# Performance work log

Measured on AMD Instinct MI355X. Metric: run time of the kernel, lower is better.

## Reference

```python
import jax, jax.numpy as jnp
import numpy as np
import math

C = 256
N_HEAD = 8
GROUPS = 16
EPS = 1e-5


def group_norm(x, w, b):
    # x: [B, C, H, W]; biased variance over (group_channels, H, W), like torch GroupNorm
    B, Cc, H, W = x.shape
    xg = x.reshape(B, GROUPS, Cc // GROUPS, H, W)
    mean = xg.mean(axis=(2, 3, 4), keepdims=True)
    var = ((xg - mean) ** 2).mean(axis=(2, 3, 4), keepdims=True)
    xn = ((xg - mean) * jax.lax.rsqrt(var + EPS)).reshape(B, Cc, H, W)
    return xn * w[None, :, None, None] + b[None, :, None, None]


def setup_inputs() -> dict:
    key = jax.random.key(0)
    k0, k1, k2, k3, k4, k5 = jax.random.split(key, 6)
    B, H, W = 4, 48, 48
    input_feat = jax.random.normal(k0, (B, C, H, W), dtype=jnp.float32)
    gn_weight = jnp.ones((C,), dtype=jnp.float32) + 0.02 * jax.random.normal(k1, (C,), dtype=jnp.float32)
    gn_bias = 0.02 * jax.random.normal(k2, (C,), dtype=jnp.float32)
    w_qkv = jax.random.normal(k3, (3 * C, C), dtype=jnp.float32) / math.sqrt(C)  # Conv2d 1x1, no bias
    w_out = jax.random.normal(k4, (C, C), dtype=jnp.float32) / math.sqrt(C)      # Conv2d 1x1
    b_out = 0.02 * jax.random.normal(k5, (C,), dtype=jnp.float32)
    return {"input_feat": input_feat, "gn_weight": gn_weight, "gn_bias": gn_bias,
            "w_qkv": w_qkv, "w_out": w_out, "b_out": b_out}


def reference(input_feat, gn_weight, gn_bias, w_qkv, w_out, b_out):
    # H=W=48 <= max_attn_size=48 -> full attention branch
    B, Cc, H, W = input_feat.shape
    n, d = N_HEAD, Cc // N_HEAD
    S = H * W
    normed = group_norm(input_feat, gn_weight, gn_bias)
    # 1x1 conv QKV: [B, 3C, H, W]
    qkv = jnp.einsum('oc,bchw->bohw', w_qkv, normed)
    # view(B, n, 3*d, H, W).chunk(3, dim=2) == reshape to (B, n, 3, d, S)
    qkv = qkv.reshape(B, n, 3, d, S)
    q, k, v = qkv[:, :, 0], qkv[:, :, 1], qkv[:, :, 2]  # each [B, n, d, S]
    # NOTE: original divides by sqrt(channel), not sqrt(head_dim)
    scale = 1.0 / math.sqrt(Cc)
    scores = jnp.einsum('bnds,bndt->bnst', q, k) * scale  # [B, n, S, S]
    attn = jax.nn.softmax(scores, axis=-1)
    o = jnp.einsum('bnst,bndt->bnds', attn, v)  # [B, n, d, S]
    o = o.reshape(B, Cc, H, W)
    out = jnp.einsum('oc,bchw->bohw', w_out, o) + b_out[None, :, None, None]
    return out + input_feat
```

## Files before the change

### kernel.cpp

```cpp
#include <hip/hip_runtime.h>
#include <hip/hip_bf16.h>
#include <stdint.h>

#define S    2304
#define CHN  256
#define BATCH 4
#define NKEYS 1152
#define QS   0.09016844005556021f

typedef __attribute__((ext_vector_type(8))) short bf16x8;
typedef __attribute__((ext_vector_type(4))) short bf16x4;
typedef __attribute__((ext_vector_type(4))) float f32x4;
typedef __attribute__((ext_vector_type(4))) uint32_t u32x4;
typedef __attribute__((ext_vector_type(4))) unsigned short u16x4;
typedef unsigned short u16;

#define AS1 __attribute__((address_space(1)))
#define AS3 __attribute__((address_space(3)))
#define GLDS(gptr, lptr) __builtin_amdgcn_global_load_lds((const AS1 void*)(gptr), (AS3 void*)(lptr), 16, 0, 0)

__device__ __forceinline__ u16 f2bf(float f) {
  union { float f; uint32_t u; } v; v.f = f;
  uint32_t u = v.u;
  u += 0x7fffu + ((u >> 16) & 1u);
  return (u16)(u >> 16);
}
__device__ __forceinline__ float bf2f(u16 h) {
  union { uint32_t u; float f; } v; v.u = ((uint32_t)h) << 16;
  return v.f;
}
__device__ __forceinline__ uint32_t pk_bf16(float a, float b) {
  union { __hip_bfloat162 h; uint32_t u; } cv;
  cv.h = __float22bfloat162_rn(make_float2(a, b));
  return cv.u;
}

__global__ void k_prep(const float* __restrict__ wq, const float* __restrict__ wo,
                       u16* __restrict__ wq_bf, u16* __restrict__ wo_bf,
                       float* __restrict__ sraw) {
  int i = blockIdx.x * 256 + threadIdx.x;
  if (blockIdx.x == 0 && threadIdx.x < 128) sraw[threadIdx.x] = 0.f;
  if (i < 768 * 256) wq_bf[i] = f2bf(wq[i]);
  int j = i - 768 * 256;
  if (j >= 0 && j < 256 * 256) wo_bf[j] = f2bf(wo[j]);
}

__global__ void k_gnstats(const float* __restrict__ x, float* __restrict__ sraw) {
  int blk = blockIdx.x;
  int bg = blk >> 2, part = blk & 3;
  const float4* p = (const float4*)(x + (size_t)bg * 36864) + part * 2304;
  float s = 0.f, ss = 0.f;
  for (int i = threadIdx.x; i < 2304; i += 256) {
    float4 v = p[i];
    s  += v.x + v.y + v.z + v.w;
    ss += v.x * v.x + v.y * v.y + v.z * v.z + v.w * v.w;
  }
  int lane = threadIdx.x & 63, wv = threadIdx.x >> 6;
  for (int m = 1; m < 64; m <<= 1) { s += __shfl_xor(s, m, 64); ss += __shfl_xor(ss, m, 64); }
  __shared__ float rs[4], rss[4];
  if (lane == 0) { rs[wv] = s; rss[wv] = ss; }
  __syncthreads();
  if (threadIdx.x == 0) {
    float S_ = rs[0] + rs[1] + rs[2] + rs[3];
    float SS = rss[0] + rss[1] + rss[2] + rss[3];
    atomicAdd(&sraw[bg * 2], S_);
    atomicAdd(&sraw[bg * 2 + 1], SS);
  }
}

__global__ void k_gnnorm(const float* __restrict__ x, const float* __restrict__ w,
                         const float* __restrict__ bias, const float* __restrict__ sraw,
                         u16* __restrict__ nt) {
  int bid = blockIdx.x;
  int b = bid / 144, r = bid % 144;
  int sblk = r >> 2, cq = r & 3;
  int t = threadIdx.x;
  int ni = t & 63, cgrp = t >> 6;
  int s = sblk * 64 + ni;
  int cbase = cq * 64 + cgrp * 16;
  int bgi = b * 16 + (cbase >> 4);
  float sx = sraw[bgi * 2], ssx = sraw[bgi * 2 + 1];
  float mean = sx * (1.f / 36864.f);
  float var  = ssx * (1.f / 36864.f) - mean * mean;
  float rstd = rsqrtf(var + 1e-5f);
  bf16x8 v0, v1;
  #pragma unroll
  for (int e = 0; e < 16; ++e) {
    int c = cbase + e;
    float val = x[(size_t)(b * 256 + c) * S + s];
    float xn = (val - mean) * rstd * w[c] + bias[c];
    if (e < 8) v0[e] = (short)f2bf(xn); else v1[e - 8] = (short)f2bf(xn);
  }
  u16* dst = nt + (size_t)(b * S + s) * 256 + cbase;
  *(bf16x8*)dst = v0;
  *(bf16x8*)(dst + 8) = v1;
}

__global__ __launch_bounds__(256) void k_qkv(const u16* __restrict__ A,
                                             const u16* __restrict__ Bm,
                                             u16* __restrict__ qkt,
                                             u16* __restrict__ vt) {
  __shared__ __align__(16) u16 As[2][64 * 32];
  __shared__ __align__(16) u16 Bs[2][128 * 32];
  int tid = threadIdx.x, lane = tid & 63, w = tid >> 6;
  int wr = w >> 1, wc = w & 1;
  int cb = lane & 15, q4 = lane >> 4;
  int m0 = blockIdx.y * 64, n0 = blockIdx.x * 128;

  const u16* gA0 = A  + (size_t)(m0 + (tid >> 2)) * 256 + (tid & 3) * 8;
  const u16* gB0 = Bm + (size_t)(n0 + (tid >> 2)) * 256 + (tid & 3) * 8;
  const u16* gB1 = gB0 + 64 * 256;
  char* lA = (char*)&As[0][0] + (w << 10);
  char* lB = (char*)&Bs[0][0] + (w << 10);

  #define STAGE_Q(buf, k0) do {                      \
    GLDS(gA0 + (k0), lA + (buf) * 4096);             \
    GLDS(gB0 + (k0), lB + (buf) * 8192);             \
    GLDS(gB1 + (k0), lB + (buf) * 8192 + 4096);      \
  } while (0)

  f32x4 zero4 = {0.f, 0.f, 0.f, 0.f};
  f32x4 acc[2][4];
  for (int i = 0; i < 2; ++i) for (int j = 0; j < 4; ++j) acc[i][j] = zero4;

  STAGE_Q(0, 0);
  __syncthreads();
  for (int ks = 0; ks < 8; ++ks) {
    int cur = ks & 1;
    if (ks < 7) STAGE_Q(cur ^ 1, (ks + 1) * 32);
    const u16* as = &As[cur][0];
    const u16* bs = &Bs[cur][0];
    bf16x8 af[2], bfr[4];
    for (int i = 0; i < 2; ++i)
      af[i]  = *(const bf16x8*)&as[(wr * 32 + i * 16 + cb) * 32 + 8 * q4];
    for (int j = 0; j < 4; ++j)
      bfr[j] = *(const bf16x8*)&bs[(wc * 64 + j * 16 + cb) * 32 + 8 * q4];
    for (int i = 0; i < 2; ++i)
      for (int j = 0; j < 4; ++j)
        acc[i][j] = __builtin_amdgcn_mfma_f32_16x16x32_bf16(af[i], bfr[j], acc[i][j], 0, 0, 0);
    __syncthreads();
  }

  for (int i = 0; i < 2; ++i)
    for (int j = 0; j < 4; ++j) {
      int ob = m0 + wr * 32 + i * 16 + q4 * 4;
      int n  = n0 + wc * 64 + j * 16 + cb;
      int h = ob / 96, oq = ob % 96;
      if (oq < 64) {
        float sc = (oq < 32) ? QS : 1.f;
        u16x4 pk;
        for (int r = 0; r < 4; ++r) pk[r] = f2bf(acc[i][j][r] * sc);
        *(u16x4*)&qkt[(size_t)n * 512 + h * 64 + oq] = pk;
      } else {
        for (int r = 0; r < 4; ++r)
          vt[(size_t)(h * 32 + oq - 64 + r) * 9216 + n] = f2bf(acc[i][j][r]);
      }
    }
  #undef STAGE_Q
}

__global__ __launch_bounds__(512) void k_attn(const u16* __restrict__ qkt,
                                              const u16* __restrict__ vt,
                                              u16* __restrict__ ot) {
  __shared__ __align__(16) u16 Ks[2][2][2048];
  __shared__ __align__(16) u16 Vd[2][2][2048];
  __shared__ float Ls[8][16];

  int tid = threadIdx.x, lane = tid & 63, w = tid >> 6;
  int cb = lane & 15, g4 = lane >> 4;
  int qw = w & 3, half = w >> 2;
  int hw = blockIdx.x;
  int orig = (hw & 7) * 144 + (hw >> 3);
  int bh = orig / 36, qtile = orig % 36;
  int b = bh >> 3, h = bh & 7;
  int q0 = qtile * 64 + qw * 16;

  const u16* kbase = qkt + (size_t)(b * S) * 512 + h * 64 + 32 + (size_t)half * NKEYS * 512;
  const u16* vbase = vt + (size_t)(h * 32) * 9216 + (size_t)b * S + half * NKEYS;

  bf16x8 qf = *(const bf16x8*)&qkt[(size_t)(b * S + q0 + cb) * 512 + h * 64 + 8 * g4];
  bf16x8 vones;
  #pragma unroll
  for (int e = 0; e < 8; ++e) vones[e] = (short)0x3F80;

  f32x4 zero4 = {0.f, 0.f, 0.f, 0.f};
  f32x4 acc_o[2]; acc_o[0] = zero4; acc_o[1] = zero4;
  f32x4 lacc4 = zero4;

  int xk = (cb ^ (cb >> 2)) & 3;

  const u16* p_k = &Ks[half][0][cb * 32 + ((g4 ^ xk) * 8)];
  const u16* p_v[2][2];
  #pragma unroll
  for (int kk = 0; kk < 2; ++kk)
    #pragma unroll
    for (int h2 = 0; h2 < 2; ++h2) {
      int chunk = 4 * kk + 2 * h2 + (g4 >> 1);
      p_v[kk][h2] = &Vd[half][0][cb * 64 + ((chunk ^ (cb & 7)) << 3) + 4 * (g4 & 1)];
    }

  int tloc = tid & 255;
  int krow = tloc >> 2, kch = (tloc & 3) ^ ((krow ^ (krow >> 2)) & 3);
  int vrow = tloc >> 3, vch = (tloc & 7) ^ (vrow & 7);
  const u16* gK = kbase + (size_t)krow * 512 + kch * 8;
  const u16* gV = vbase + (size_t)vrow * 9216 + vch * 8;
  char* ldsK = (char*)&Ks[half][0][0] + (qw << 10);
  char* ldsV = (char*)&Vd[half][0][0] + (qw << 10);

  #define STAGE_A(buf) do {                          \
    GLDS(gK, ldsK + (buf) * 4096);                   \
    GLDS(gV, ldsV + (buf) * 4096);                   \
    gK += 64 * 512; gV += 64;                        \
  } while (0)

  #define TILE(buf, pf) do {                                                   \
    if (pf) STAGE_A(buf ^ 1);                                                  \
    bf16x8 kf[4];                                                              \
    _Pragma("unroll")                                                          \
    for (int k4 = 0; k4 < 4; ++k4)                                             \
      kf[k4] = *(const bf16x8*)(p_k + (buf) * 2048 + k4 * 512);                \
    bf16x4 vlo[2][2], vhi[2][2];                                 \
    _Pragma("unroll")                                                          \
    for (int jd = 0; jd < 2; ++jd)                                             \
      _Pragma("unroll")                                                        \
      for (int kk = 0; kk < 2; ++kk) {                                         \
        vlo[jd][kk] = *(const bf16x4*)(p_v[kk][0] + (buf) * 2048 + jd * 1024); \
        vhi[jd][kk] = *(const bf16x4*)(p_v[kk][1] + (buf) * 2048 + jd * 1024); \
      }                                                                        \
    f32x4 pacc[4];                                                             \
    __builtin_amdgcn_s_setprio(1);                                             \
    _Pragma("unroll")                                                          \
    for (int k4 = 0; k4 < 4; ++k4)                                             \
      pacc[k4] = __builtin_amdgcn_mfma_f32_16x16x32_bf16(kf[k4], qf, zero4, 0, 0, 0); \
    __builtin_amdgcn_s_setprio(0);                                             \
    uint32_t W01[4], W23[4];                                                   \
    _Pragma("unroll")                                                          \
    for (int k4 = 0; k4 < 4; ++k4) {                                           \
      f32x4 p = pacc[k4];                                                      \
      float e0 = __builtin_amdgcn_exp2f(p[0]);                                 \
      float e1 = __builtin_amdgcn_exp2f(p[1]);                                 \
      float e2 = __builtin_amdgcn_exp2f(p[2]);                                 \
      float e3 = __builtin_amdgcn_exp2f(p[3]);                                 \
      W01[k4] = pk_bf16(e0, e1);                                               \
      W23[k4] = pk_bf16(e2, e3);                                               \
    }                                                                          \
    union { u32x4 u; bf16x8 v; } pu0, pu1;                                     \
    pu0.u = (u32x4){W01[0], W23[0], W01[1], W23[1]};                           \
    pu1.u = (u32x4){W01[2], W23[2], W01[3], W23[3]};                           \
    __builtin_amdgcn_s_setprio(1);                                             \
    lacc4 = __builtin_amdgcn_mfma_f32_16x16x32_bf16(pu0.v, vones, lacc4, 0, 0, 0); \
    lacc4 = __builtin_amdgcn_mfma_f32_16x16x32_bf16(pu1.v, vones, lacc4, 0, 0, 0); \
    _Pragma("unroll")                                                          \
    for (int jd = 0; jd < 2; ++jd) {                                           \
      bf16x8 vb0 = __builtin_shufflevector(vlo[jd][0], vhi[jd][0], 0,1,2,3,4,5,6,7); \
      bf16x8 vb1 = __builtin_shufflevector(vlo[jd][1], vhi[jd][1], 0,1,2,3,4,5,6,7); \
      acc_o[jd] = __builtin_amdgcn_mfma_f32_16x16x32_bf16(pu0.v, vb0, acc_o[jd], 0, 0, 0); \
      acc_o[jd] = __builtin_amdgcn_mfma_f32_16x16x32_bf16(pu1.v, vb1, acc_o[jd], 0, 0, 0); \
    }                                                                          \
    __builtin_amdgcn_s_setprio(0);                                             \
    __syncthreads();                                                           \
  } while (0)

  STAGE_A(0);
  __syncthreads();
  for (int it = 0; it < 9; ++it) {
    TILE(0, 1);
    TILE(1, it < 8);
  }

  float* OsF = (float*)&Ks[0][0][0];
  float* myO = OsF + w * 512;
  #pragma unroll
  for (int jd = 0; jd < 2; ++jd)
    *(f32x4*)&myO[(cb + 16 * jd) * 16 + 4 * g4] = acc_o[jd];
  if (cb == 0)
    *(f32x4*)&Ls[w][4 * g4] = lacc4;
  __syncthreads();

  const float* A0 = OsF + qw * 512;
  const float* A1 = OsF + (qw + 4) * 512;
  int dd = half * 16 + cb;
  f32x4 s0 = *(const f32x4*)&A0[dd * 16 + 4 * g4];
  f32x4 s1 = *(const f32x4*)&A1[dd * 16 + 4 * g4];
  f32x4 lt0 = *(const f32x4*)&Ls[qw][4 * g4];
  f32x4 lt1 = *(const f32x4*)&Ls[qw + 4][4 * g4];
  #pragma unroll
  for (int r = 0; r < 4; ++r) {
    float inv = __builtin_amdgcn_rcpf(lt0[r] + lt1[r]);
    int sq = q0 + 4 * g4 + r;
    ot[(size_t)(b * S + sq) * 256 + h * 32 + dd] = f2bf((s0[r] + s1[r]) * inv);
  }
  #undef STAGE_A
  #undef TILE
}

__global__ __launch_bounds__(256) void k_oproj(const u16* __restrict__ A,
                                               const u16* __restrict__ Bm,
                                               float* __restrict__ out,
                                               const float* __restrict__ bias,
                                               const float* __restrict__ resid) {
  __shared__ __align__(16) u16 As[2][64 * 32];
  __shared__ __align__(16) u16 Bs[2][64 * 32];
  int tid = threadIdx.x, lane = tid & 63, w = tid >> 6;
  int cb = lane & 15, q4 = lane >> 4;
  int m0 = blockIdx.y * 64, n0 = blockIdx.x * 64;

  const u16* gA0 = A  + (size_t)(m0 + (tid >> 2)) * 256 + (tid & 3) * 8;
  const u16* gB0 = Bm + (size_t)(n0 + (tid >> 2)) * 256 + (tid & 3) * 8;
  char* lA = (char*)&As[0][0] + (w << 10);
  char* lB = (char*)&Bs[0][0] + (w << 10);

  #define STAGE_O(buf, k0) do {                      \
    GLDS(gA0 + (k0), lA + (buf) * 4096);             \
    GLDS(gB0 + (k0), lB + (buf) * 4096);             \
  } while (0)

  f32x4 zero4 = {0.f, 0.f, 0.f, 0.f};
  f32x4 acc[4];
  for (int j = 0; j < 4; ++j) acc[j] = zero4;

  STAGE_O(0, 0);
  __syncthreads();
  for (int ks = 0; ks < 8; ++ks) {
    int cur = ks & 1;
    if (ks < 7) STAGE_O(cur ^ 1, (ks + 1) * 32);
    const u16* as = &As[cur][0];
    const u16* bs = &Bs[cur][0];
    bf16x8 af = *(const bf16x8*)&as[(w * 16 + cb) * 32 + 8 * q4];
    bf16x8 bfr[4];
    for (int j = 0; j < 4; ++j)
      bfr[j] = *(const bf16x8*)&bs[(j * 16 + cb) * 32 + 8 * q4];
    for (int j = 0; j < 4; ++j)
      acc[j] = __builtin_amdgcn_mfma_f32_16x16x32_bf16(af, bfr[j], acc[j], 0, 0, 0);
    __syncthreads();
  }

  for (int j = 0; j < 4; ++j)
    for (int r = 0; r < 4; ++r) {
      int o = m0 + w * 16 + q4 * 4 + r;
      int n = n0 + j * 16 + cb;
      int b = n / S, s2 = n % S;
      size_t gi = (size_t)(b * 256 + o) * S + s2;
      out[gi] = acc[j][r] + bias[o] + resid[gi];
    }
  #undef STAGE_O
}

extern "C" void kernel_launch(void* const* d_in, const int* in_sizes, int n_in,
                              void* d_out, int out_size, void* d_ws, size_t ws_size,
                              hipStream_t stream) {
  const float* input = (const float*)d_in[0];
  const float* gnw   = (const float*)d_in[1];
  const float* gnb   = (const float*)d_in[2];
  const float* wqkv  = (const float*)d_in[3];
  const float* wout  = (const float*)d_in[4];
  const float* bout  = (const float*)d_in[5];
  float* out = (float*)d_out;
  char* ws = (char*)d_ws;

  size_t o_wq  = 0;
  size_t o_wo  = o_wq + (size_t)768 * 256 * 2;
  size_t o_st  = o_wo + (size_t)256 * 256 * 2;
  size_t o_nt  = o_st + 1024;
  size_t o_qkt = o_nt + (size_t)9216 * 256 * 2;
  size_t o_vt  = o_qkt + (size_t)9216 * 512 * 2;

  u16*    wq_bf = (u16*)(ws + o_wq);
  u16*    wo_bf = (u16*)(ws + o_wo);
  float*  sraw  = (float*)(ws + o_st);
  u16*    nt    = (u16*)(ws + o_nt);
  u16*    qkt   = (u16*)(ws + o_qkt);
  u16*    vt    = (u16*)(ws + o_vt);
  u16*    otb   = (u16*)(ws + o_nt);

  k_prep<<<1024, 256, 0, stream>>>(wqkv, wout, wq_bf, wo_bf, sraw);
  k_gnstats<<<256, 256, 0, stream>>>(input, sraw);
  k_gnnorm<<<576, 256, 0, stream>>>(input, gnw, gnb, sraw, nt);
  k_qkv<<<dim3(72, 12), 256, 0, stream>>>(wq_bf, nt, qkt, vt);
  k_attn<<<1152, 512, 0, stream>>>(qkt, vt, otb);
  k_oproj<<<dim3(144, 4), 256, 0, stream>>>(wo_bf, otb, out, bout, input);
}
```

Before: 88.03 us.

## Drop intra-block key split in attention kernel, use 256-thread blocks

The attention kernel no longer splits the key range across two halves of a 512-thread block. Each 256-thread block now walks all 2304 keys itself, which removes the LDS partial-sum exchange, the extra barrier and the final combine step. The kernel runs twice as many tile iterations per wave and asks for higher occupancy through launch bounds (256, 8). The trade-off is less parallelism per query tile and a longer serial loop, in exchange for less LDS use and simpler synchronisation.

Result: slower. 90.28 us (+2.6%).

```diff
diff --git a/kernel.cpp b/kernel.cpp
--- a/kernel.cpp
+++ b/kernel.cpp
@@ -5,7 +5,6 @@
 #define S    2304
 #define CHN  256
 #define BATCH 4
-#define NKEYS 1152
 #define QS   0.09016844005556021f
 
 typedef __attribute__((ext_vector_type(8))) short bf16x8;
@@ -159,24 +158,22 @@
   #undef STAGE_Q
 }
 
-__global__ __launch_bounds__(512) void k_attn(const u16* __restrict__ qkt,
-                                              const u16* __restrict__ vt,
-                                              u16* __restrict__ ot) {
-  __shared__ __align__(16) u16 Ks[2][2][2048];
-  __shared__ __align__(16) u16 Vd[2][2][2048];
-  __shared__ float Ls[8][16];
+__global__ __launch_bounds__(256, 8) void k_attn(const u16* __restrict__ qkt,
+                                                 const u16* __restrict__ vt,
+                                                 u16* __restrict__ ot) {
+  __shared__ __align__(16) u16 Ks[2][2048];
+  __shared__ __align__(16) u16 Vd[2][2048];
 
   int tid = threadIdx.x, lane = tid & 63, w = tid >> 6;
   int cb = lane & 15, g4 = lane >> 4;
-  int qw = w & 3, half = w >> 2;
   int hw = blockIdx.x;
   int orig = (hw & 7) * 144 + (hw >> 3);
   int bh = orig / 36, qtile = orig % 36;
   int b = bh >> 3, h = bh & 7;
-  int q0 = qtile * 64 + qw * 16;
-
-  const u16* kbase = qkt + (size_t)(b * S) * 512 + h * 64 + 32 + (size_t)half * NKEYS * 512;
-  const u16* vbase = vt + (size_t)(h * 32) * 9216 + (size_t)b * S + half * NKEYS;
+  int q0 = qtile * 64 + w * 16;
+
+  const u16* kbase = qkt + (size_t)(b * S) * 512 + h * 64 + 32;
+  const u16* vbase = vt + (size_t)(h * 32) * 9216 + (size_t)b * S;
 
   bf16x8 qf = *(const bf16x8*)&qkt[(size_t)(b * S + q0 + cb) * 512 + h * 64 + 8 * g4];
   bf16x8 vones;
@@ -189,23 +186,22 @@
 
   int xk = (cb ^ (cb >> 2)) & 3;
 
-  const u16* p_k = &Ks[half][0][cb * 32 + ((g4 ^ xk) * 8)];
+  const u16* p_k = &Ks[0][cb * 32 + ((g4 ^ xk) * 8)];
   const u16* p_v[2][2];
   #pragma unroll
   for (int kk = 0; kk < 2; ++kk)
     #pragma unroll
     for (int h2 = 0; h2 < 2; ++h2) {
       int chunk = 4 * kk + 2 * h2 + (g4 >> 1);
-      p_v[kk][h2] = &Vd[half][0][cb * 64 + ((chunk ^ (cb & 7)) << 3) + 4 * (g4 & 1)];
+      p_v[kk][h2] = &Vd[0][cb * 64 + ((chunk ^ (cb & 7)) << 3) + 4 * (g4 & 1)];
     }
 
-  int tloc = tid & 255;
-  int krow = tloc >> 2, kch = (tloc & 3) ^ ((krow ^ (krow >> 2)) & 3);
-  int vrow = tloc >> 3, vch = (tloc & 7) ^ (vrow & 7);
+  int krow = tid >> 2, kch = (tid & 3) ^ ((krow ^ (krow >> 2)) & 3);
+  int vrow = tid >> 3, vch = (tid & 7) ^ (vrow & 7);
   const u16* gK = kbase + (size_t)krow * 512 + kch * 8;
   const u16* gV = vbase + (size_t)vrow * 9216 + vch * 8;
-  char* ldsK = (char*)&Ks[half][0][0] + (qw << 10);
-  char* ldsV = (char*)&Vd[half][0][0] + (qw << 10);
+  char* ldsK = (char*)&Ks[0][0] + (w << 10);
+  char* ldsV = (char*)&Vd[0][0] + (w << 10);
 
   #define STAGE_A(buf) do {                          \
     GLDS(gK, ldsK + (buf) * 4096);                   \
@@ -263,32 +259,18 @@
 
   STAGE_A(0);
   __syncthreads();
-  for (int it = 0; it < 9; ++it) {
+  for (int it = 0; it < 18; ++it) {
     TILE(0, 1);
-    TILE(1, it < 8);
-  }
-
-  float* OsF = (float*)&Ks[0][0][0];
-  float* myO = OsF + w * 512;
-  #pragma unroll
-  for (int jd = 0; jd < 2; ++jd)
-    *(f32x4*)&myO[(cb + 16 * jd) * 16 + 4 * g4] = acc_o[jd];
-  if (cb == 0)
-    *(f32x4*)&Ls[w][4 * g4] = lacc4;
-  __syncthreads();
-
-  const float* A0 = OsF + qw * 512;
-  const float* A1 = OsF + (qw + 4) * 512;
-  int dd = half * 16 + cb;
-  f32x4 s0 = *(const f32x4*)&A0[dd * 16 + 4 * g4];
-  f32x4 s1 = *(const f32x4*)&A1[dd * 16 + 4 * g4];
-  f32x4 lt0 = *(const f32x4*)&Ls[qw][4 * g4];
-  f32x4 lt1 = *(const f32x4*)&Ls[qw + 4][4 * g4];
+    TILE(1, it < 17);
+  }
+
   #pragma unroll
   for (int r = 0; r < 4; ++r) {
-    float inv = __builtin_amdgcn_rcpf(lt0[r] + lt1[r]);
+    float inv = __builtin_amdgcn_rcpf(lacc4[r]);
     int sq = q0 + 4 * g4 + r;
-    ot[(size_t)(b * S + sq) * 256 + h * 32 + dd] = f2bf((s0[r] + s1[r]) * inv);
+    #pragma unroll
+    for (int jd = 0; jd < 2; ++jd)
+      ot[(size_t)(b * S + sq) * 256 + h * 32 + cb + 16 * jd] = f2bf(acc_o[jd][r] * inv);
   }
   #undef STAGE_A
   #undef TILE
@@ -377,6 +359,6 @@
   k_gnstats<<<256, 256, 0, stream>>>(input, sraw);
   k_gnnorm<<<576, 256, 0, stream>>>(input, gnw, gnb, sraw, nt);
   k_qkv<<<dim3(72, 12), 256, 0, stream>>>(wq_bf, nt, qkt, vt);
-  k_attn<<<1152, 512, 0, stream>>>(qkt, vt, otb);
+  k_attn<<<1152, 256, 0, stream>>>(qkt, vt, otb);
   k_oproj<<<dim3(144, 4), 256, 0, stream>>>(wo_bf, otb, out, bout, input);
 }
```
